# Kernel tuning notes

Hardware: AMD Instinct MI355X
Metric: run time of the kernel (lower is better)

The kernel has to match this reference:

```python
import jax, jax.numpy as jnp
import numpy as np
import math

D_MODEL = 1024
NUM_HEADS = 16
D_HEAD = 64
K_EIG = 16
B, N = 4, 4096


def setup_inputs() -> dict:
    key = jax.random.key(0)
    ks = jax.random.split(key, 8)
    s = 1.0 / math.sqrt(D_MODEL)
    return {
        "x": jax.random.normal(ks[0], (B, N, D_MODEL), jnp.float32),
        "Wq": jax.random.normal(ks[1], (D_MODEL, NUM_HEADS * D_HEAD), jnp.float32) * s,
        "bq": jnp.zeros((NUM_HEADS * D_HEAD,), jnp.float32),
        "Wk": jax.random.normal(ks[2], (D_MODEL, NUM_HEADS * D_HEAD), jnp.float32) * s,
        "bk": jnp.zeros((NUM_HEADS * D_HEAD,), jnp.float32),
        "Wv": jax.random.normal(ks[3], (D_MODEL, NUM_HEADS * D_HEAD), jnp.float32) * s,
        "bv": jnp.zeros((NUM_HEADS * D_HEAD,), jnp.float32),
        "eigenvectors": jax.random.normal(ks[4], (NUM_HEADS, K_EIG), jnp.float32),
        "filter_weights": jnp.ones((K_EIG,), jnp.float32),
    }


def reference(x, Wq, bq, Wk, bk, Wv, bv, eigenvectors, filter_weights):
    Bb, Nn, _ = x.shape
    H, Dh = NUM_HEADS, D_HEAD
    # projections -> [B,N,H,Dh]
    Q = (x @ Wq + bq).reshape(Bb, Nn, H, Dh)
    K = (x @ Wk + bk).reshape(Bb, Nn, H, Dh)
    V = (x @ Wv + bv).reshape(Bb, Nn, H, Dh)
    # head axis -> eigen (frequency) axis: [B,N,K,Dh]
    Qf = jnp.einsum('hk,bnhd->bnkd', eigenvectors, Q)
    Kf = jnp.einsum('hk,bnhd->bnkd', eigenvectors, K)
    Vf = jnp.einsum('hk,bnhd->bnkd', eigenvectors, V)
    # learnable spectral filter, broadcast over eigen axis
    w = filter_weights[None, None, :, None]
    Qf = Qf * w
    Kf = Kf * w
    Vf = Vf * w
    # small k x k attention per token
    scores = jnp.einsum('bnkd,bnld->bnkl', Qf, Kf) / math.sqrt(Dh)
    attn = jax.nn.softmax(scores, axis=-1)  # dropout is identity in eval
    out_f = jnp.einsum('bnkl,bnld->bnkd', attn, Vf)
    # back to head space: [B,N,H,Dh]
    out = jnp.einsum('hk,bnkd->bnhd', eigenvectors, out_f)
    return out.reshape(Bb, Nn, H * Dh)
```

## Files before the change

kernel.cpp:

```cpp
#include <hip/hip_runtime.h>
#include <stdint.h>

#define NTOK   16384
#define DM     1024
#define NQKV   3072

typedef __attribute__((ext_vector_type(8))) _Float16 half8;
typedef __attribute__((ext_vector_type(4))) _Float16 half4;
typedef __attribute__((ext_vector_type(4))) float    float4v;

#define MFMA16 __builtin_amdgcn_mfma_f32_16x16x32_f16
#define BARX()  do{ asm volatile("" ::: "memory"); __builtin_amdgcn_s_barrier(); asm volatile("" ::: "memory"); }while(0)
#define VMCNT(N) asm volatile("s_waitcnt vmcnt(" #N ")" ::: "memory")

__device__ __forceinline__ void async_cp16(const void* g, void* l){
  __builtin_amdgcn_global_load_lds(
      (const __attribute__((address_space(1))) void*)g,
      (__attribute__((address_space(3))) void*)l, 16, 0, 0);
}

__global__ void cvt_x_kernel(const float* __restrict__ x, _Float16* __restrict__ xb){
  int i = (blockIdx.x * blockDim.x + threadIdx.x) * 8;
  const int stride = gridDim.x * blockDim.x * 8;
  for(; i < NTOK * DM; i += stride){
    float4v v0 = *(const float4v*)(x + i);
    float4v v1 = *(const float4v*)(x + i + 4);
    half8 o;
    o[0]=(_Float16)v0[0]; o[1]=(_Float16)v0[1]; o[2]=(_Float16)v0[2]; o[3]=(_Float16)v0[3];
    o[4]=(_Float16)v1[0]; o[5]=(_Float16)v1[1]; o[6]=(_Float16)v1[2]; o[7]=(_Float16)v1[3];
    *(half8*)(xb + i) = o;
  }
}

__global__ __launch_bounds__(256)
void prep_w_kernel(const float* __restrict__ Wq, const float* __restrict__ Wk,
                   const float* __restrict__ Wv, const float* __restrict__ E,
                   const float* __restrict__ fw, _Float16* __restrict__ WT){
  __shared__ float Wl[8][1032];
  __shared__ float oT[16][8][65];
  __shared__ float sEv[256];
  __shared__ float sFw[16];
  const int t  = threadIdx.x;
  const int bx = blockIdx.x;
  const int p  = bx >> 7, rt = bx & 127;
  const int c0 = rt * 8;
  const float* W = (p == 0) ? Wq : (p == 1) ? Wk : Wv;
  sEv[t] = E[t];
  if(t < 16) sFw[t] = fw[t];

  #pragma unroll
  for(int j = 0; j < 32; ++j){
    const int flat = j * 256 + t;
    const int row = flat >> 10, col = flat & 1023;
    Wl[row][col] = W[(size_t)(c0 + row) * 1024 + col];
  }
  __syncthreads();

  const int d = t & 63, rg = t >> 6;
  #pragma unroll
  for(int rr = 0; rr < 2; ++rr){
    const int row = rg * 2 + rr;
    float w[16];
    #pragma unroll
    for(int h = 0; h < 16; ++h) w[h] = Wl[row][h * 64 + d];
    #pragma unroll
    for(int ke = 0; ke < 16; ++ke){
      float acc = 0.f;
      #pragma unroll
      for(int h = 0; h < 16; ++h) acc += sEv[h * 16 + ke] * w[h];
      oT[ke][row][d] = acc * sFw[ke];
    }
  }
  __syncthreads();

  #pragma unroll
  for(int k4 = 0; k4 < 4; ++k4){
    const int idx = k4 * 256 + t;
    const int ke = idx >> 6, dd = idx & 63;
    half8 o;
    #pragma unroll
    for(int c = 0; c < 8; ++c) o[c] = (_Float16)oT[ke][c][dd];
    const int n = (p * 16 + ke) * 64 + dd;
    *(half8*)(WT + (size_t)n * 1024 + c0) = o;
  }
}

__global__ void prep_b_kernel(const float* __restrict__ bq, const float* __restrict__ bk,
                              const float* __restrict__ bv, const float* __restrict__ E,
                              const float* __restrict__ fw, float* __restrict__ fb){
  const int n = blockIdx.x * blockDim.x + threadIdx.x;
  if(n >= NQKV) return;
  const int p = n >> 10, kE = (n >> 6) & 15, d = n & 63;
  const float* b = (p == 0) ? bq : (p == 1) ? bk : bv;
  float acc = 0.f;
  for(int h = 0; h < 16; ++h) acc += E[h * 16 + kE] * b[h * 64 + d];
  fb[n] = acc * fw[kE];
}

struct FlagF { static constexpr bool value = false; };
struct FlagT { static constexpr bool value = true; };

__global__ __launch_bounds__(512, 2)
void gemm_qkv_kernel(const _Float16* __restrict__ A,
                     const _Float16* __restrict__ BT,
                     const float* __restrict__ bias,
                     _Float16* __restrict__ C){
  extern __shared__ _Float16 lds[];
  const int t = threadIdx.x;
  const int lane = t & 63, wv = t >> 6;
  const int l15 = lane & 15, q = lane >> 4;
  const int wr = wv >> 2, wc = wv & 3;

  const int bid = blockIdx.x;
  const int xcd = bid & 7, s = bid >> 3;
  const int mt = xcd * 8 + (s & 7);
  const int nt = s >> 3;
  const int m0 = mt * 256, n0 = nt * 256;

  const int stR = wv * 16 + (lane >> 3);
  const int stC = (((lane & 7) ^ (lane >> 3)) * 8);
  const int stD = (wv * 128 + lane) * 8;
  const int qsw = (q * 8) ^ ((l15 & 7) * 8);
  const int aoffb = (wr * 16 + l15) * 64;
  const int boffb = (wc * 16 + l15) * 64;

  auto stgA = [&](_Float16* nb, int kc, int h){
    const _Float16* g = A + (size_t)(m0 + h * 128 + stR) * 1024 + kc + stC;
    _Float16* d = nb + h * 8192 + stD;
    async_cp16(g, d);
    async_cp16(g + 8 * 1024, d + 512);
  };
  auto stgB = [&](_Float16* nb, int kc, int h){
    const _Float16* g = BT + (size_t)(n0 + h * 128 + stR) * 1024 + kc + stC;
    _Float16* d = nb + 16384 + h * 8192 + stD;
    async_cp16(g, d);
    async_cp16(g + 8 * 1024, d + 512);
  };

  float4v acc[8][4];
  #pragma unroll
  for(int m = 0; m < 8; ++m)
    #pragma unroll
    for(int n = 0; n < 4; ++n){ acc[m][n][0]=0.f; acc[m][n][1]=0.f; acc[m][n][2]=0.f; acc[m][n][3]=0.f; }

  stgA(lds, 0, 0);
  stgB(lds, 0, 0);
  stgB(lds, 0, 1);
  stgA(lds, 0, 1);
  VMCNT(0);
  BARX();

  int kt = 0;
  auto ktile = [&](auto lastc){
    constexpr bool LAST = decltype(lastc)::value;
    const _Float16* pA = lds + (kt & 1) * 32768;
    const _Float16* pB = pA + 16384;
    _Float16* nxt = lds + ((kt + 1) & 1) * 32768;
    const int kn = (kt + 1) * 64;

    half8 a0[8], b0[4];
    half8 a1[8], b1[4];

    #pragma unroll
    for(int m = 0; m < 8; ++m) a0[m] = *(const half8*)(pA + aoffb + m * 2048 + qsw);
    #pragma unroll
    for(int n = 0; n < 4; ++n) b0[n] = *(const half8*)(pB + boffb + n * 4096 + qsw);
    if constexpr(!LAST){ stgA(nxt, kn, 0); stgA(nxt, kn, 1); }

    __builtin_amdgcn_s_setprio(1);
    #pragma unroll
    for(int m = 0; m < 4; ++m)
      #pragma unroll
      for(int n = 0; n < 4; ++n)
        acc[m][n] = MFMA16(a0[m], b0[n], acc[m][n], 0, 0, 0);
    __builtin_amdgcn_s_setprio(0);

    #pragma unroll
    for(int m = 0; m < 8; ++m) a1[m] = *(const half8*)(pA + aoffb + m * 2048 + (qsw ^ 32));
    #pragma unroll
    for(int n = 0; n < 4; ++n) b1[n] = *(const half8*)(pB + boffb + n * 4096 + (qsw ^ 32));
    if constexpr(!LAST){ stgB(nxt, kn, 0); stgB(nxt, kn, 1); }

    __builtin_amdgcn_s_setprio(1);
    #pragma unroll
    for(int m = 4; m < 8; ++m)
      #pragma unroll
      for(int n = 0; n < 4; ++n)
        acc[m][n] = MFMA16(a0[m], b0[n], acc[m][n], 0, 0, 0);

    #pragma unroll
    for(int m = 0; m < 8; ++m)
      #pragma unroll
      for(int n = 0; n < 4; ++n)
        acc[m][n] = MFMA16(a1[m], b1[n], acc[m][n], 0, 0, 0);
    __builtin_amdgcn_s_setprio(0);

    if constexpr(!LAST){
      VMCNT(0);
      BARX();
    }
  };

  for(kt = 0; kt < 15; ++kt) ktile(FlagF{});
  ktile(FlagT{});

  #pragma unroll
  for(int n = 0; n < 4; ++n){
    const int col = n0 + (n * 4 + wc) * 16 + l15;
    const float bs = bias[col];
    #pragma unroll
    for(int m = 0; m < 8; ++m){
      const int rbase = m0 + (m * 2 + wr) * 16 + q * 4;
      #pragma unroll
      for(int r = 0; r < 4; ++r)
        C[(size_t)(rbase + r) * NQKV + col] = (_Float16)(acc[m][n][r] + bs);
    }
  }
}

__global__ __launch_bounds__(256)
void attn_kernel(const _Float16* __restrict__ QKV,
                 const float* __restrict__ E,
                 float* __restrict__ out){
  __shared__ _Float16 sV[4 * 1024];
  __shared__ _Float16 sE[16 * 32];
  __shared__ _Float16 pT[4][16 * 32];
  __shared__ _Float16 gT[4][16 * 32];

  const int t = threadIdx.x, lane = t & 63, wv = t >> 6;
  const int l15 = lane & 15, q = lane >> 4;

  {
    #pragma unroll
    for(int s = 0; s < 2; ++s){
      const int idx = s * 256 + t;
      const int row = idx >> 5, col = idx & 31;
      sE[idx] = (col < 16) ? (_Float16)E[row * 16 + col] : (_Float16)0.f;
    }
    #pragma unroll
    for(int s = 0; s < 4; ++s){
      const int idx = s * 256 + t;
      const int w = idx >> 8, rem = idx & 255;
      const int off = (rem >> 4) * 32 + 16 + (rem & 15);
      pT[w][off] = (_Float16)0.f;
      gT[w][off] = (_Float16)0.f;
    }
  }

  const _Float16* gb = QKV + (size_t)blockIdx.x * (4 * 3072);
  #pragma unroll
  for(int i = 0; i < 2; ++i){
    const int f = i * 256 + t;
    async_cp16(gb + (f >> 7) * 3072 + 2048 + (f & 127) * 8, sV + f * 8);
  }

  const int tok = blockIdx.x * 4 + wv;
  const _Float16* tg = QKV + (size_t)tok * 3072;

  half8 aK0 = *(const half8*)(tg + 1024 + l15 * 64 + q * 8);
  half8 aK1 = *(const half8*)(tg + 1024 + l15 * 64 + 32 + q * 8);
  half8 bQ0 = *(const half8*)(tg + l15 * 64 + q * 8);
  half8 bQ1 = *(const half8*)(tg + l15 * 64 + 32 + q * 8);
  float4v S; S[0]=0.f; S[1]=0.f; S[2]=0.f; S[3]=0.f;
  S = __builtin_amdgcn_mfma_f32_16x16x32_f16(aK0, bQ0, S, 0, 0, 0);
  S = __builtin_amdgcn_mfma_f32_16x16x32_f16(aK1, bQ1, S, 0, 0, 0);

  float v[4];
  #pragma unroll
  for(int r = 0; r < 4; ++r) v[r] = S[r] * 0.125f;
  float mx = fmaxf(fmaxf(v[0], v[1]), fmaxf(v[2], v[3]));
  mx = fmaxf(mx, __shfl_xor(mx, 16));
  mx = fmaxf(mx, __shfl_xor(mx, 32));
  float e[4];
  #pragma unroll
  for(int r = 0; r < 4; ++r) e[r] = __expf(v[r] - mx);
  float sm = (e[0] + e[1]) + (e[2] + e[3]);
  sm += __shfl_xor(sm, 16);
  sm += __shfl_xor(sm, 32);
  const float rs = 1.f / sm;

  __syncthreads();

  _Float16* pw = pT[wv];
  #pragma unroll
  for(int r = 0; r < 4; ++r) pw[(q * 4 + r) * 32 + l15] = (_Float16)(e[r] * rs);
  half8 bP = *(const half8*)(pw + l15 * 32 + q * 8);
  half8 aE = *(const half8*)(sE + l15 * 32 + q * 8);

  float4v G; G[0]=0.f; G[1]=0.f; G[2]=0.f; G[3]=0.f;
  G = __builtin_amdgcn_mfma_f32_16x16x32_f16(aE, bP, G, 0, 0, 0);

  _Float16* gw = gT[wv];
  #pragma unroll
  for(int r = 0; r < 4; ++r) gw[(q * 4 + r) * 32 + l15] = (_Float16)G[r];
  half8 aG = *(const half8*)(gw + l15 * 32 + q * 8);

  const _Float16* vb = sV + wv * 1024 + (q & 1) * 8 * 64;
  float* ob = out + (size_t)tok * 1024;
  #pragma unroll
  for(int tt = 0; tt < 4; ++tt){
    half8 vf;
    #pragma unroll
    for(int jj = 0; jj < 8; ++jj) vf[jj] = vb[jj * 64 + tt * 16 + l15];
    float4v O; O[0]=0.f; O[1]=0.f; O[2]=0.f; O[3]=0.f;
    O = __builtin_amdgcn_mfma_f32_16x16x32_f16(aG, vf, O, 0, 0, 0);
    #pragma unroll
    for(int r = 0; r < 4; ++r)
      ob[(q * 4 + r) * 64 + tt * 16 + l15] = O[r];
  }
}

extern "C" void kernel_launch(void* const* d_in, const int* in_sizes, int n_in,
                              void* d_out, int out_size, void* d_ws, size_t ws_size,
                              hipStream_t stream){
  const float* x  = (const float*)d_in[0];
  const float* Wq = (const float*)d_in[1];
  const float* bq = (const float*)d_in[2];
  const float* Wk = (const float*)d_in[3];
  const float* bk = (const float*)d_in[4];
  const float* Wv = (const float*)d_in[5];
  const float* bv = (const float*)d_in[6];
  const float* E  = (const float*)d_in[7];
  const float* fw = (const float*)d_in[8];
  float* out = (float*)d_out;

  char* ws = (char*)d_ws;
  _Float16* xb  = (_Float16*)ws;
  _Float16* WT  = (_Float16*)(ws + (size_t)32 * 1024 * 1024);
  float*    fb  = (float*)   (ws + (size_t)39 * 1024 * 1024);
  _Float16* QKV = (_Float16*)(ws + (size_t)40 * 1024 * 1024);

  static bool attr_done = false;
  if(!attr_done){
    hipFuncSetAttribute((const void*)gemm_qkv_kernel,
                        hipFuncAttributeMaxDynamicSharedMemorySize, 131072);
    attr_done = true;
  }

  hipLaunchKernelGGL(cvt_x_kernel, dim3(2048), dim3(256), 0, stream, x, xb);
  hipLaunchKernelGGL(prep_w_kernel, dim3(384), dim3(256), 0, stream, Wq, Wk, Wv, E, fw, WT);
  hipLaunchKernelGGL(prep_b_kernel, dim3(12), dim3(256), 0, stream, bq, bk, bv, E, fw, fb);
  hipLaunchKernelGGL(gemm_qkv_kernel, dim3(768), dim3(512), 131072, stream, xb, WT, fb, QKV);
  hipLaunchKernelGGL(attn_kernel, dim3(NTOK / 4), dim3(256), 0, stream, QKV, E, out);
}
```

Before: 284.3 us.

## Store V transposed from GEMM to load MFMA operands directly, drop LDS staging

The weight-prep and bias kernels now permute the V third of the fused QKV projection so that V is written in a d-major, eigen-minor layout. The attention kernel can then fetch each MFMA B operand as one contiguous half8 global load into registers. This replaces the async LDS copy of V, the per-element strided LDS gathers, the shared eigenvector staging, and the block-wide __syncthreads. The eigenvector operand is loaded straight from global memory per wave, and the zero-padding writes are made per-wave. The aim is less LDS traffic and no block synchronisation in a kernel dominated by memory, at the cost of more redundant small global loads per wave.

```diff
diff --git a/kernel.cpp b/kernel.cpp
--- a/kernel.cpp
+++ b/kernel.cpp
@@ -80,7 +80,7 @@
     half8 o;
     #pragma unroll
     for(int c = 0; c < 8; ++c) o[c] = (_Float16)oT[ke][c][dd];
-    const int n = (p * 16 + ke) * 64 + dd;
+    const int n = (p == 2) ? (2048 + dd * 16 + ke) : (p * 1024 + ke * 64 + dd);
     *(half8*)(WT + (size_t)n * 1024 + c0) = o;
   }
 }
@@ -90,7 +90,10 @@
                               const float* __restrict__ fw, float* __restrict__ fb){
   const int n = blockIdx.x * blockDim.x + threadIdx.x;
   if(n >= NQKV) return;
-  const int p = n >> 10, kE = (n >> 6) & 15, d = n & 63;
+  const int p = n >> 10;
+  int kE, d;
+  if(p == 2){ kE = n & 15; d = (n >> 4) & 63; }
+  else      { kE = (n >> 6) & 15; d = n & 63; }
   const float* b = (p == 0) ? bq : (p == 1) ? bk : bv;
   float acc = 0.f;
   for(int h = 0; h < 16; ++h) acc += E[h * 16 + kE] * b[h * 64 + d];
@@ -222,37 +225,11 @@
 void attn_kernel(const _Float16* __restrict__ QKV,
                  const float* __restrict__ E,
                  float* __restrict__ out){
-  __shared__ _Float16 sV[4 * 1024];
-  __shared__ _Float16 sE[16 * 32];
   __shared__ _Float16 pT[4][16 * 32];
   __shared__ _Float16 gT[4][16 * 32];
 
   const int t = threadIdx.x, lane = t & 63, wv = t >> 6;
   const int l15 = lane & 15, q = lane >> 4;
-
-  {
-    #pragma unroll
-    for(int s = 0; s < 2; ++s){
-      const int idx = s * 256 + t;
-      const int row = idx >> 5, col = idx & 31;
-      sE[idx] = (col < 16) ? (_Float16)E[row * 16 + col] : (_Float16)0.f;
-    }
-    #pragma unroll
-    for(int s = 0; s < 4; ++s){
-      const int idx = s * 256 + t;
-      const int w = idx >> 8, rem = idx & 255;
-      const int off = (rem >> 4) * 32 + 16 + (rem & 15);
-      pT[w][off] = (_Float16)0.f;
-      gT[w][off] = (_Float16)0.f;
-    }
-  }
-
-  const _Float16* gb = QKV + (size_t)blockIdx.x * (4 * 3072);
-  #pragma unroll
-  for(int i = 0; i < 2; ++i){
-    const int f = i * 256 + t;
-    async_cp16(gb + (f >> 7) * 3072 + 2048 + (f & 127) * 8, sV + f * 8);
-  }
 
   const int tok = blockIdx.x * 4 + wv;
   const _Float16* tg = QKV + (size_t)tok * 3072;
@@ -261,9 +238,33 @@
   half8 aK1 = *(const half8*)(tg + 1024 + l15 * 64 + 32 + q * 8);
   half8 bQ0 = *(const half8*)(tg + l15 * 64 + q * 8);
   half8 bQ1 = *(const half8*)(tg + l15 * 64 + 32 + q * 8);
+  const _Float16* tv = tg + 2048;
+  half8 vf[4];
+  #pragma unroll
+  for(int tt = 0; tt < 4; ++tt)
+    vf[tt] = *(const half8*)(tv + (tt * 16 + l15) * 16 + (q & 1) * 8);
+  half8 aE;
+  if(q < 2){
+    float4v e0 = *(const float4v*)(E + l15 * 16 + q * 8);
+    float4v e1 = *(const float4v*)(E + l15 * 16 + q * 8 + 4);
+    aE[0]=(_Float16)e0[0]; aE[1]=(_Float16)e0[1]; aE[2]=(_Float16)e0[2]; aE[3]=(_Float16)e0[3];
+    aE[4]=(_Float16)e1[0]; aE[5]=(_Float16)e1[1]; aE[6]=(_Float16)e1[2]; aE[7]=(_Float16)e1[3];
+  }else{
+    aE[0]=(_Float16)0.f; aE[1]=(_Float16)0.f; aE[2]=(_Float16)0.f; aE[3]=(_Float16)0.f;
+    aE[4]=(_Float16)0.f; aE[5]=(_Float16)0.f; aE[6]=(_Float16)0.f; aE[7]=(_Float16)0.f;
+  }
+
+  #pragma unroll
+  for(int s = 0; s < 4; ++s){
+    const int idx = s * 64 + lane;
+    const int off = (idx >> 4) * 32 + 16 + (idx & 15);
+    pT[wv][off] = (_Float16)0.f;
+    gT[wv][off] = (_Float16)0.f;
+  }
+
   float4v S; S[0]=0.f; S[1]=0.f; S[2]=0.f; S[3]=0.f;
-  S = __builtin_amdgcn_mfma_f32_16x16x32_f16(aK0, bQ0, S, 0, 0, 0);
-  S = __builtin_amdgcn_mfma_f32_16x16x32_f16(aK1, bQ1, S, 0, 0, 0);
+  S = MFMA16(aK0, bQ0, S, 0, 0, 0);
+  S = MFMA16(aK1, bQ1, S, 0, 0, 0);
 
   float v[4];
   #pragma unroll
@@ -279,31 +280,24 @@
   sm += __shfl_xor(sm, 32);
   const float rs = 1.f / sm;
 
-  __syncthreads();
-
   _Float16* pw = pT[wv];
   #pragma unroll
   for(int r = 0; r < 4; ++r) pw[(q * 4 + r) * 32 + l15] = (_Float16)(e[r] * rs);
   half8 bP = *(const half8*)(pw + l15 * 32 + q * 8);
-  half8 aE = *(const half8*)(sE + l15 * 32 + q * 8);
 
   float4v G; G[0]=0.f; G[1]=0.f; G[2]=0.f; G[3]=0.f;
-  G = __builtin_amdgcn_mfma_f32_16x16x32_f16(aE, bP, G, 0, 0, 0);
+  G = MFMA16(aE, bP, G, 0, 0, 0);
 
   _Float16* gw = gT[wv];
   #pragma unroll
   for(int r = 0; r < 4; ++r) gw[(q * 4 + r) * 32 + l15] = (_Float16)G[r];
   half8 aG = *(const half8*)(gw + l15 * 32 + q * 8);
 
-  const _Float16* vb = sV + wv * 1024 + (q & 1) * 8 * 64;
   float* ob = out + (size_t)tok * 1024;
   #pragma unroll
   for(int tt = 0; tt < 4; ++tt){
-    half8 vf;
-    #pragma unroll
-    for(int jj = 0; jj < 8; ++jj) vf[jj] = vb[jj * 64 + tt * 16 + l15];
     float4v O; O[0]=0.f; O[1]=0.f; O[2]=0.f; O[3]=0.f;
-    O = __builtin_amdgcn_mfma_f32_16x16x32_f16(aG, vf, O, 0, 0, 0);
+    O = MFMA16(aG, vf[tt], O, 0, 0, 0);
     #pragma unroll
     for(int r = 0; r < 4; ++r)
       ob[(q * 4 + r) * 64 + tt * 16 + l15] = O[r];
```

New measurement: 286.0 us. About the same (+0.6%).
